# Kernel optimization log

Hardware: AMD Instinct MI355X
Metric: run time of the kernel (lower is better)

The kernel has to match this reference:

```python
import jax, jax.numpy as jnp
import numpy as np

NEG_SLOPE = 0.01  # torch F.leaky_relu default

def _leaky(x):
    return jnp.where(x >= 0, x, NEG_SLOPE * x)

def _gcn(x, W, b, src, dst, w, n):
    # GCNConv(add_self_loops=False, normalize=False):
    # h = x @ W; out[dst] += w * h[src]; out += b
    h = x @ W
    agg = jax.ops.segment_sum(w[:, None] * h[src], dst, num_segments=n)
    return agg + b

def setup_inputs() -> dict:
    key = jax.random.key(0)
    ks = jax.random.split(key, 10)
    N, E, IN, HID, OUT, B = 100000, 300000, 256, 256, 256, 128
    features = jax.random.normal(ks[0], (N, IN), dtype=jnp.float32)
    values = jax.random.uniform(ks[1], (E,), dtype=jnp.float32)
    s = 1.0 / np.sqrt(IN)
    W1 = jax.random.normal(ks[2], (IN, HID), dtype=jnp.float32) * s
    b1 = jnp.zeros((HID,), dtype=jnp.float32)
    W2 = jax.random.normal(ks[3], (HID + IN, OUT), dtype=jnp.float32) * (1.0 / np.sqrt(HID + IN))
    b2 = jnp.zeros((OUT,), dtype=jnp.float32)
    Wl = jax.random.normal(ks[4], (HID + OUT, IN), dtype=jnp.float32) * (1.0 / np.sqrt(HID + OUT))
    bl = jnp.zeros((IN,), dtype=jnp.float32)
    adjs = jax.random.randint(ks[5], (2, E), 0, N, dtype=jnp.int64)
    batch = jnp.sort(jax.random.randint(ks[6], (N,), 0, B, dtype=jnp.int64))
    root_idx = jax.random.randint(ks[7], (B,), 0, N, dtype=jnp.int64)
    return {"features": features, "values": values, "W1": W1, "b1": b1,
            "W2": W2, "b2": b2, "Wl": Wl, "bl": bl,
            "adjs": adjs, "batch": batch, "root_idx": root_idx}

def reference(features, values, W1, b1, W2, b2, Wl, bl, adjs, batch, root_idx):
    N = features.shape[0]
    src, dst = adjs[0], adjs[1]
    f1 = features  # [N, in]
    h = _gcn(f1, W1, b1, src, dst, values, N)  # conv1 -> [N, hid]
    f2 = h
    # root_extend: per-batch broadcast of root features == gather f1[root_idx[batch]]
    root1 = f1[root_idx[batch]]  # [N, in]
    x = _leaky(jnp.concatenate([h, root1], axis=1))
    # dropout is identity at inference
    x = _gcn(x, W2, b2, src, dst, values, N)  # conv2 -> [N, out]
    x = _leaky(x)
    root2 = f2[root_idx[batch]]  # [N, hid]
    x = jnp.concatenate([x, root2], axis=1)
    return _leaky(x @ Wl + bl)  # [N, in]
```

## Files before the change

kernel.cpp:

```cpp
#include <hip/hip_runtime.h>

typedef short short8 __attribute__((ext_vector_type(8)));
typedef float floatx4 __attribute__((ext_vector_type(4)));

#define LEAKY(v) ((v) >= 0.0f ? (v) : 0.01f * (v))

constexpr int D = 256;

__device__ __forceinline__ short f2bf(float x) {
  unsigned u = __float_as_uint(x);
  u += 0x7fffu + ((u >> 16) & 1u);
  return (short)(u >> 16);
}
__device__ __forceinline__ float bf2f(short s) {
  return __uint_as_float(((unsigned)(unsigned short)s) << 16);
}

#define AS1 __attribute__((address_space(1)))
#define AS3 __attribute__((address_space(3)))

__device__ __forceinline__ void gload_lds16(const void* g, void* lds) {
  __builtin_amdgcn_global_load_lds((const AS1 void*)g, (AS3 void*)lds, 16, 0, 0);
}

__global__ void transpose_w(const float* __restrict__ W1,
                            const float* __restrict__ W2,
                            const float* __restrict__ Wl,
                            short* __restrict__ Wt) {
  __shared__ float t[32][33];
  const float* src = (blockIdx.z == 0) ? W1 : (blockIdx.z == 1) ? W2 : Wl;
  short* dst = Wt + (size_t)blockIdx.z * D * D;
  int tx = threadIdx.x, ty = threadIdx.y;
  t[ty][tx] = src[(size_t)(blockIdx.y * 32 + ty) * D + blockIdx.x * 32 + tx];
  __syncthreads();
  dst[(size_t)(blockIdx.x * 32 + ty) * D + blockIdx.y * 32 + tx] =
      f2bf(t[tx][ty]);
}

__global__ __launch_bounds__(256) void conv_bf(const float* __restrict__ X,
                                               short* __restrict__ Y,
                                               long n8) {
  long i = (long)blockIdx.x * 256 + threadIdx.x;
  const long stride = (long)gridDim.x * 256;
  for (; i < n8; i += stride) {
    float4 v0 = ((const float4*)X)[2 * i];
    float4 v1 = ((const float4*)X)[2 * i + 1];
    short8 s;
    s[0] = f2bf(v0.x); s[1] = f2bf(v0.y); s[2] = f2bf(v0.z); s[3] = f2bf(v0.w);
    s[4] = f2bf(v1.x); s[5] = f2bf(v1.y); s[6] = f2bf(v1.z); s[7] = f2bf(v1.w);
    ((short8*)Y)[i] = s;
  }
}

template <bool ADD_ROW, bool FINAL>
__global__ __launch_bounds__(512, 2) void gemm_pipe(
    const short* __restrict__ A, const short* __restrict__ Wt,
    const float* __restrict__ R, const int* __restrict__ batch,
    const float* __restrict__ bias, void* __restrict__ Cvoid, int M,
    int nTiles) {
  __shared__ __align__(16) short As[2][32 * 256];
  const int tid = threadIdx.x;
  const int l = tid & 63, w = tid >> 6, lm = l & 15, q = l >> 4;
  const int ncol0 = w * 32;

  short8 bf[2][8];
#pragma unroll
  for (int j = 0; j < 2; j++)
#pragma unroll
    for (int kk = 0; kk < 8; kk++)
      bf[j][kk] = *(const short8*)(Wt + (size_t)(ncol0 + j * 16 + lm) * D +
                                   kk * 32 + q * 8);
#pragma unroll
  for (int j = 0; j < 2; j++)
#pragma unroll
    for (int kk = 0; kk < 8; kk++)
      asm volatile("" : "+v"(bf[j][kk]));

  float4 b4[2];
  if (FINAL) {
#pragma unroll
    for (int j = 0; j < 2; j++)
      b4[j] = *(const float4*)(bias + ncol0 + j * 16 + q * 4);
  }

  const int stride = gridDim.x;
  int t = blockIdx.x;
  int p = 0;

  auto stage = [&](int tile, int buf) {
#pragma unroll
    for (int r = 0; r < 2; r++) {
      const int s = r * 8 + w;
      const int kk = s >> 1, i = s & 1;
      int grow = tile * 32 + i * 16 + lm;
      grow = grow < M ? grow : M - 1;
      const char* src = (const char*)A + (size_t)grow * 512 + kk * 64 + q * 16;
      gload_lds16(src, (char*)(&As[buf][0]) + s * 1024);
    }
  };

  if (t < nTiles) stage(t, 0);

  for (; t < nTiles; t += stride) {
    __syncthreads();
    const int nxt = t + stride;
    if (nxt < nTiles) stage(nxt, p ^ 1);

    floatx4 acc[2][2];
#pragma unroll
    for (int i = 0; i < 2; i++)
#pragma unroll
      for (int j = 0; j < 2; j++) acc[i][j] = (floatx4){0.f, 0.f, 0.f, 0.f};

    const char* base = (const char*)(&As[p][0]) + (size_t)l * 16;
#pragma unroll
    for (int kk = 0; kk < 8; kk++) {
      short8 a[2];
#pragma unroll
      for (int i = 0; i < 2; i++)
        a[i] = *(const short8*)(base + (kk * 2 + i) * 1024);
#pragma unroll
      for (int i = 0; i < 2; i++)
#pragma unroll
        for (int j = 0; j < 2; j++)
          acc[i][j] = __builtin_amdgcn_mfma_f32_16x16x32_bf16(
              bf[j][kk], a[i], acc[i][j], 0, 0, 0);
    }

    const int rowBase = t * 32;
#pragma unroll
    for (int i = 0; i < 2; i++) {
      const int row = rowBase + i * 16 + lm;
      if (row < M) {
        int rb = 0;
        if (ADD_ROW) rb = batch[row];
#pragma unroll
        for (int j = 0; j < 2; j++) {
          const int col0 = ncol0 + j * 16 + q * 4;
          float c0 = acc[i][j][0], c1 = acc[i][j][1], c2 = acc[i][j][2],
                c3 = acc[i][j][3];
          if (ADD_ROW) {
            float4 rv = *(const float4*)(R + (size_t)rb * D + col0);
            c0 += rv.x; c1 += rv.y; c2 += rv.z; c3 += rv.w;
          }
          if (!FINAL) {
            uint2 o;
            o.x = (unsigned)(unsigned short)f2bf(c0) |
                  ((unsigned)(unsigned short)f2bf(c1) << 16);
            o.y = (unsigned)(unsigned short)f2bf(c2) |
                  ((unsigned)(unsigned short)f2bf(c3) << 16);
            *(uint2*)((short*)Cvoid + (size_t)row * D + col0) = o;
          } else {
            c0 += b4[j].x; c1 += b4[j].y; c2 += b4[j].z; c3 += b4[j].w;
            c0 = LEAKY(c0); c1 = LEAKY(c1); c2 = LEAKY(c2); c3 = LEAKY(c3);
            float4 o = {c0, c1, c2, c3};
            *(float4*)((float*)Cvoid + (size_t)row * D + col0) = o;
          }
        }
      }
    }
    p ^= 1;
  }
}

__global__ void count_dst(const int* __restrict__ dst, int* __restrict__ offs,
                          int E) {
  int e = blockIdx.x * 256 + threadIdx.x;
  if (e < E) atomicAdd(&offs[dst[e]], 1);
}

__global__ void scan_blocks(int* __restrict__ offs, int* __restrict__ bsums,
                            int n) {
  __shared__ int tmp[256];
  int i = blockIdx.x * 256 + threadIdx.x;
  int v = (i < n) ? offs[i] : 0;
  tmp[threadIdx.x] = v;
  __syncthreads();
  for (int off = 1; off < 256; off <<= 1) {
    int t = (threadIdx.x >= off) ? tmp[threadIdx.x - off] : 0;
    __syncthreads();
    tmp[threadIdx.x] += t;
    __syncthreads();
  }
  if (i < n) offs[i] = tmp[threadIdx.x] - v;
  if (threadIdx.x == 255) bsums[blockIdx.x] = tmp[255];
}

__global__ void scan_sums(int* __restrict__ bs, int nb) {
  __shared__ int tmp[1024];
  int v = (threadIdx.x < nb) ? bs[threadIdx.x] : 0;
  tmp[threadIdx.x] = v;
  __syncthreads();
  for (int off = 1; off < 1024; off <<= 1) {
    int t = (threadIdx.x >= off) ? tmp[threadIdx.x - off] : 0;
    __syncthreads();
    tmp[threadIdx.x] += t;
    __syncthreads();
  }
  if (threadIdx.x < nb) bs[threadIdx.x] = tmp[threadIdx.x] - v;
}

__global__ void add_offsets(int* __restrict__ offs, const int* __restrict__ bs,
                            int n, int* __restrict__ cursor) {
  int i = blockIdx.x * 256 + threadIdx.x;
  if (i < n) {
    int o = offs[i] + bs[blockIdx.x];
    offs[i] = o;
    cursor[i] = o;
  }
}

__global__ void fill_buckets(const int* __restrict__ src,
                             const int* __restrict__ dst,
                             const float* __restrict__ vals,
                             int* __restrict__ cursor, int* __restrict__ esrc,
                             float* __restrict__ ew, int E) {
  int e = blockIdx.x * 256 + threadIdx.x;
  if (e < E) {
    int p = atomicAdd(&cursor[dst[e]], 1);
    esrc[p] = src[e];
    ew[p] = vals[e];
  }
}

__global__ __launch_bounds__(256) void aggregate_bf(
    const short* __restrict__ H, const int* __restrict__ offs,
    const int* __restrict__ esrc, const float* __restrict__ ew,
    const float* __restrict__ bias, short* __restrict__ out, int N, int E) {
  int node = blockIdx.x * 4 + (threadIdx.x >> 6);
  if (node >= N) return;
  int lane = threadIdx.x & 63;
  int beg = offs[node];
  int end = (node == N - 1) ? E : offs[node + 1];
  float a0 = 0.f, a1 = 0.f, a2 = 0.f, a3 = 0.f;
  int i = beg;
  for (; i + 1 < end; i += 2) {
    int s0 = esrc[i], s1 = esrc[i + 1];
    float w0 = ew[i], w1 = ew[i + 1];
    uint2 p0 = ((const uint2*)(H + (size_t)s0 * D))[lane];
    uint2 p1 = ((const uint2*)(H + (size_t)s1 * D))[lane];
    a0 += w0 * bf2f((short)(p0.x & 0xffff)) + w1 * bf2f((short)(p1.x & 0xffff));
    a1 += w0 * bf2f((short)(p0.x >> 16))    + w1 * bf2f((short)(p1.x >> 16));
    a2 += w0 * bf2f((short)(p0.y & 0xffff)) + w1 * bf2f((short)(p1.y & 0xffff));
    a3 += w0 * bf2f((short)(p0.y >> 16))    + w1 * bf2f((short)(p1.y >> 16));
  }
  if (i < end) {
    int s = esrc[i];
    float wv = ew[i];
    uint2 pk = ((const uint2*)(H + (size_t)s * D))[lane];
    a0 += wv * bf2f((short)(pk.x & 0xffff));
    a1 += wv * bf2f((short)(pk.x >> 16));
    a2 += wv * bf2f((short)(pk.y & 0xffff));
    a3 += wv * bf2f((short)(pk.y >> 16));
  }
  float4 b = ((const float4*)bias)[lane];
  a0 = LEAKY(a0 + b.x);
  a1 = LEAKY(a1 + b.y);
  a2 = LEAKY(a2 + b.z);
  a3 = LEAKY(a3 + b.w);
  uint2 o;
  o.x = (unsigned)(unsigned short)f2bf(a0) |
        ((unsigned)(unsigned short)f2bf(a1) << 16);
  o.y = (unsigned)(unsigned short)f2bf(a2) |
        ((unsigned)(unsigned short)f2bf(a3) << 16);
  ((uint2*)(out + (size_t)node * D))[lane] = o;
}

__global__ void root_both(const float* __restrict__ X,
                          const int* __restrict__ root_idx,
                          const float* __restrict__ W2, float* __restrict__ R1,
                          const short* __restrict__ H,
                          const int* __restrict__ offs,
                          const int* __restrict__ esrc,
                          const float* __restrict__ ew,
                          const float* __restrict__ b1,
                          const float* __restrict__ Wl, float* __restrict__ R2,
                          int N, int E, int B) {
  __shared__ float a[D];
  int j = threadIdx.x;
  if ((int)blockIdx.x < B) {
    int b = blockIdx.x;
    int r = root_idx[b];
    a[j] = LEAKY(X[(size_t)r * D + j]);
    __syncthreads();
    float acc = 0.f;
#pragma unroll 8
    for (int k = 0; k < D; k++) acc += a[k] * W2[(size_t)(D + k) * D + j];
    R1[b * D + j] = acc;
  } else {
    int b = blockIdx.x - B;
    int r = root_idx[b];
    int beg = offs[r], end = (r == N - 1) ? E : offs[r + 1];
    float acc = b1[j];
    for (int e = beg; e < end; e++)
      acc += ew[e] * bf2f(H[(size_t)esrc[e] * D + j]);
    a[j] = acc;
    __syncthreads();
    float s = 0.f;
#pragma unroll 8
    for (int k = 0; k < D; k++) s += a[k] * Wl[(size_t)(D + k) * D + j];
    R2[b * D + j] = s;
  }
}

extern "C" void kernel_launch(void* const* d_in, const int* in_sizes, int n_in,
                              void* d_out, int out_size, void* d_ws,
                              size_t ws_size, hipStream_t stream) {
  const float* features = (const float*)d_in[0];
  const float* values   = (const float*)d_in[1];
  const float* W1 = (const float*)d_in[2];
  const float* b1 = (const float*)d_in[3];
  const float* W2 = (const float*)d_in[4];
  const float* b2 = (const float*)d_in[5];
  const float* Wl = (const float*)d_in[6];
  const float* bl = (const float*)d_in[7];
  const int* adjs = (const int*)d_in[8];
  const int* batch = (const int*)d_in[9];
  const int* root_idx = (const int*)d_in[10];

  const int N = in_sizes[0] / D;
  const int E = in_sizes[1];
  const int B = in_sizes[10];
  const int* srcI = adjs;
  const int* dstI = adjs + E;

  short* bf0 = (short*)d_ws;
  short* bf1 = bf0 + (size_t)N * D;
  short* Wt = bf1 + (size_t)N * D;
  float* R1 = (float*)(Wt + (size_t)3 * D * D);
  float* R2 = R1 + (size_t)B * D;
  float* ew = R2 + (size_t)B * D;
  int* offs = (int*)(ew + E);
  int* cursor = offs + N;
  int* esrc = cursor + N;
  int* bsums = esrc + E;

  const int nb = (N + 255) / 256;

  hipMemsetAsync(offs, 0, (size_t)N * sizeof(int), stream);
  count_dst<<<(E + 255) / 256, 256, 0, stream>>>(dstI, offs, E);
  scan_blocks<<<nb, 256, 0, stream>>>(offs, bsums, N);
  scan_sums<<<1, 1024, 0, stream>>>(bsums, nb);
  add_offsets<<<nb, 256, 0, stream>>>(offs, bsums, N, cursor);
  fill_buckets<<<(E + 255) / 256, 256, 0, stream>>>(srcI, dstI, values, cursor,
                                                    esrc, ew, E);

  transpose_w<<<dim3(8, 8, 3), dim3(32, 32), 0, stream>>>(W1, W2, Wl, Wt);

  conv_bf<<<2048, 256, 0, stream>>>(features, bf1, (long)N * D / 8);

  const int nTiles = (N + 31) / 32;
  const int ggrid = 512;
  const int aggGrid = (N + 3) / 4;

  gemm_pipe<false, false><<<ggrid, 512, 0, stream>>>(
      bf1, Wt, nullptr, nullptr, nullptr, bf0, N, nTiles);

  aggregate_bf<<<aggGrid, 256, 0, stream>>>(bf0, offs, esrc, ew, b1, bf1, N, E);

  root_both<<<2 * B, 256, 0, stream>>>(features, root_idx, W2, R1, bf0, offs,
                                       esrc, ew, b1, Wl, R2, N, E, B);

  gemm_pipe<true, false><<<ggrid, 512, 0, stream>>>(
      bf1, Wt + (size_t)D * D, R1, batch, nullptr, bf0, N, nTiles);

  aggregate_bf<<<aggGrid, 256, 0, stream>>>(bf0, offs, esrc, ew, b2, bf1, N, E);

  gemm_pipe<true, true><<<ggrid, 512, 0, stream>>>(
      bf1, Wt + (size_t)2 * D * D, R2, batch, bl, (float*)d_out, N, nTiles);
}
```

Before: 434.2 us.

## Fuse fp32-to-bf16 conversion into first GEMM and widen aggregate loads

Removes the separate conversion kernel by letting the first GEMM stream fp32 features straight into LDS and convert them to bf16 when it builds the MFMA operands. This drops a full write and re-read of an N×256 bf16 buffer, but doubles the LDS tile size for that GEMM, which may lower occupancy. The aggregation kernel also now has each half-wave process a different edge with 16-byte loads and combines the two halves with a cross-lane shuffle, so each wave keeps two edge gathers in flight.

```diff
diff --git a/kernel.cpp b/kernel.cpp
--- a/kernel.cpp
+++ b/kernel.cpp
@@ -37,28 +37,14 @@
       f2bf(t[tx][ty]);
 }
 
-__global__ __launch_bounds__(256) void conv_bf(const float* __restrict__ X,
-                                               short* __restrict__ Y,
-                                               long n8) {
-  long i = (long)blockIdx.x * 256 + threadIdx.x;
-  const long stride = (long)gridDim.x * 256;
-  for (; i < n8; i += stride) {
-    float4 v0 = ((const float4*)X)[2 * i];
-    float4 v1 = ((const float4*)X)[2 * i + 1];
-    short8 s;
-    s[0] = f2bf(v0.x); s[1] = f2bf(v0.y); s[2] = f2bf(v0.z); s[3] = f2bf(v0.w);
-    s[4] = f2bf(v1.x); s[5] = f2bf(v1.y); s[6] = f2bf(v1.z); s[7] = f2bf(v1.w);
-    ((short8*)Y)[i] = s;
-  }
-}
-
-template <bool ADD_ROW, bool FINAL>
+template <bool A_F32, bool ADD_ROW, bool FINAL>
 __global__ __launch_bounds__(512, 2) void gemm_pipe(
-    const short* __restrict__ A, const short* __restrict__ Wt,
+    const void* __restrict__ Avoid, const short* __restrict__ Wt,
     const float* __restrict__ R, const int* __restrict__ batch,
     const float* __restrict__ bias, void* __restrict__ Cvoid, int M,
     int nTiles) {
-  __shared__ __align__(16) short As[2][32 * 256];
+  constexpr int TB = A_F32 ? 32768 : 16384;
+  __shared__ __align__(16) char As[2][TB];
   const int tid = threadIdx.x;
   const int l = tid & 63, w = tid >> 6, lm = l & 15, q = l >> 4;
   const int ncol0 = w * 32;
@@ -88,14 +74,29 @@
   int p = 0;
 
   auto stage = [&](int tile, int buf) {
-#pragma unroll
-    for (int r = 0; r < 2; r++) {
-      const int s = r * 8 + w;
-      const int kk = s >> 1, i = s & 1;
-      int grow = tile * 32 + i * 16 + lm;
-      grow = grow < M ? grow : M - 1;
-      const char* src = (const char*)A + (size_t)grow * 512 + kk * 64 + q * 16;
-      gload_lds16(src, (char*)(&As[buf][0]) + s * 1024);
+    if (A_F32) {
+#pragma unroll
+      for (int r = 0; r < 4; r++) {
+        const int c = r * 8 + w;
+        const int s = c >> 1, h = c & 1;
+        const int kk = s >> 1, i = s & 1;
+        int grow = tile * 32 + i * 16 + lm;
+        grow = grow < M ? grow : M - 1;
+        const char* src = (const char*)Avoid + (size_t)grow * 1024 +
+                          kk * 128 + q * 32 + h * 16;
+        gload_lds16(src, &As[buf][s * 2048 + h * 1024]);
+      }
+    } else {
+#pragma unroll
+      for (int r = 0; r < 2; r++) {
+        const int s = r * 8 + w;
+        const int kk = s >> 1, i = s & 1;
+        int grow = tile * 32 + i * 16 + lm;
+        grow = grow < M ? grow : M - 1;
+        const char* src =
+            (const char*)Avoid + (size_t)grow * 512 + kk * 64 + q * 16;
+        gload_lds16(src, &As[buf][s * 1024]);
+      }
     }
   };
 
@@ -112,13 +113,24 @@
 #pragma unroll
       for (int j = 0; j < 2; j++) acc[i][j] = (floatx4){0.f, 0.f, 0.f, 0.f};
 
-    const char* base = (const char*)(&As[p][0]) + (size_t)l * 16;
+    const char* base = &As[p][0] + (size_t)l * 16;
 #pragma unroll
     for (int kk = 0; kk < 8; kk++) {
       short8 a[2];
 #pragma unroll
-      for (int i = 0; i < 2; i++)
-        a[i] = *(const short8*)(base + (kk * 2 + i) * 1024);
+      for (int i = 0; i < 2; i++) {
+        if (A_F32) {
+          const int s = kk * 2 + i;
+          float4 lo = *(const float4*)(base + s * 2048);
+          float4 hi = *(const float4*)(base + s * 2048 + 1024);
+          short8 sv;
+          sv[0] = f2bf(lo.x); sv[1] = f2bf(lo.y); sv[2] = f2bf(lo.z); sv[3] = f2bf(lo.w);
+          sv[4] = f2bf(hi.x); sv[5] = f2bf(hi.y); sv[6] = f2bf(hi.z); sv[7] = f2bf(hi.w);
+          a[i] = sv;
+        } else {
+          a[i] = *(const short8*)(base + (kk * 2 + i) * 1024);
+        }
+      }
 #pragma unroll
       for (int i = 0; i < 2; i++)
 #pragma unroll
@@ -229,41 +241,49 @@
     const float* __restrict__ bias, short* __restrict__ out, int N, int E) {
   int node = blockIdx.x * 4 + (threadIdx.x >> 6);
   if (node >= N) return;
-  int lane = threadIdx.x & 63;
+  const int lane = threadIdx.x & 63;
+  const int half = lane >> 5, li = lane & 31;
   int beg = offs[node];
   int end = (node == N - 1) ? E : offs[node + 1];
-  float a0 = 0.f, a1 = 0.f, a2 = 0.f, a3 = 0.f;
-  int i = beg;
-  for (; i + 1 < end; i += 2) {
-    int s0 = esrc[i], s1 = esrc[i + 1];
-    float w0 = ew[i], w1 = ew[i + 1];
-    uint2 p0 = ((const uint2*)(H + (size_t)s0 * D))[lane];
-    uint2 p1 = ((const uint2*)(H + (size_t)s1 * D))[lane];
-    a0 += w0 * bf2f((short)(p0.x & 0xffff)) + w1 * bf2f((short)(p1.x & 0xffff));
-    a1 += w0 * bf2f((short)(p0.x >> 16))    + w1 * bf2f((short)(p1.x >> 16));
-    a2 += w0 * bf2f((short)(p0.y & 0xffff)) + w1 * bf2f((short)(p1.y & 0xffff));
-    a3 += w0 * bf2f((short)(p0.y >> 16))    + w1 * bf2f((short)(p1.y >> 16));
-  }
-  if (i < end) {
-    int s = esrc[i];
-    float wv = ew[i];
-    uint2 pk = ((const uint2*)(H + (size_t)s * D))[lane];
+  float a0 = 0.f, a1 = 0.f, a2 = 0.f, a3 = 0.f, a4 = 0.f, a5 = 0.f,
+        a6 = 0.f, a7 = 0.f;
+  for (int i = beg; i < end; i += 2) {
+    const int idx = i + half;
+    const bool v = idx < end;
+    int s = esrc[v ? idx : i];
+    float wv = v ? ew[idx] : 0.f;
+    uint4 pk = *(const uint4*)(H + (size_t)s * D + li * 8);
     a0 += wv * bf2f((short)(pk.x & 0xffff));
     a1 += wv * bf2f((short)(pk.x >> 16));
     a2 += wv * bf2f((short)(pk.y & 0xffff));
     a3 += wv * bf2f((short)(pk.y >> 16));
-  }
-  float4 b = ((const float4*)bias)[lane];
-  a0 = LEAKY(a0 + b.x);
-  a1 = LEAKY(a1 + b.y);
-  a2 = LEAKY(a2 + b.z);
-  a3 = LEAKY(a3 + b.w);
-  uint2 o;
-  o.x = (unsigned)(unsigned short)f2bf(a0) |
-        ((unsigned)(unsigned short)f2bf(a1) << 16);
-  o.y = (unsigned)(unsigned short)f2bf(a2) |
-        ((unsigned)(unsigned short)f2bf(a3) << 16);
-  ((uint2*)(out + (size_t)node * D))[lane] = o;
+    a4 += wv * bf2f((short)(pk.z & 0xffff));
+    a5 += wv * bf2f((short)(pk.z >> 16));
+    a6 += wv * bf2f((short)(pk.w & 0xffff));
+    a7 += wv * bf2f((short)(pk.w >> 16));
+  }
+  a0 += __shfl_xor(a0, 32); a1 += __shfl_xor(a1, 32);
+  a2 += __shfl_xor(a2, 32); a3 += __shfl_xor(a3, 32);
+  a4 += __shfl_xor(a4, 32); a5 += __shfl_xor(a5, 32);
+  a6 += __shfl_xor(a6, 32); a7 += __shfl_xor(a7, 32);
+  if (half == 0) {
+    float4 b0 = *(const float4*)(bias + li * 8);
+    float4 b1 = *(const float4*)(bias + li * 8 + 4);
+    a0 = LEAKY(a0 + b0.x); a1 = LEAKY(a1 + b0.y);
+    a2 = LEAKY(a2 + b0.z); a3 = LEAKY(a3 + b0.w);
+    a4 = LEAKY(a4 + b1.x); a5 = LEAKY(a5 + b1.y);
+    a6 = LEAKY(a6 + b1.z); a7 = LEAKY(a7 + b1.w);
+    uint4 o;
+    o.x = (unsigned)(unsigned short)f2bf(a0) |
+          ((unsigned)(unsigned short)f2bf(a1) << 16);
+    o.y = (unsigned)(unsigned short)f2bf(a2) |
+          ((unsigned)(unsigned short)f2bf(a3) << 16);
+    o.z = (unsigned)(unsigned short)f2bf(a4) |
+          ((unsigned)(unsigned short)f2bf(a5) << 16);
+    o.w = (unsigned)(unsigned short)f2bf(a6) |
+          ((unsigned)(unsigned short)f2bf(a7) << 16);
+    *(uint4*)(out + (size_t)node * D + li * 8) = o;
+  }
 }
 
 __global__ void root_both(const float* __restrict__ X,
@@ -347,25 +367,23 @@
 
   transpose_w<<<dim3(8, 8, 3), dim3(32, 32), 0, stream>>>(W1, W2, Wl, Wt);
 
-  conv_bf<<<2048, 256, 0, stream>>>(features, bf1, (long)N * D / 8);
-
   const int nTiles = (N + 31) / 32;
   const int ggrid = 512;
   const int aggGrid = (N + 3) / 4;
 
-  gemm_pipe<false, false><<<ggrid, 512, 0, stream>>>(
-      bf1, Wt, nullptr, nullptr, nullptr, bf0, N, nTiles);
+  gemm_pipe<true, false, false><<<ggrid, 512, 0, stream>>>(
+      features, Wt, nullptr, nullptr, nullptr, bf0, N, nTiles);
 
   aggregate_bf<<<aggGrid, 256, 0, stream>>>(bf0, offs, esrc, ew, b1, bf1, N, E);
 
   root_both<<<2 * B, 256, 0, stream>>>(features, root_idx, W2, R1, bf0, offs,
                                        esrc, ew, b1, Wl, R2, N, E, B);
 
-  gemm_pipe<true, false><<<ggrid, 512, 0, stream>>>(
+  gemm_pipe<false, true, false><<<ggrid, 512, 0, stream>>>(
       bf1, Wt + (size_t)D * D, R1, batch, nullptr, bf0, N, nTiles);
 
   aggregate_bf<<<aggGrid, 256, 0, stream>>>(bf0, offs, esrc, ew, b2, bf1, N, E);
 
-  gemm_pipe<true, true><<<ggrid, 512, 0, stream>>>(
+  gemm_pipe<false, true, true><<<ggrid, 512, 0, stream>>>(
       bf1, Wt + (size_t)2 * D * D, R2, batch, bl, (float*)d_out, N, nTiles);
 }
```

Result: faster. 419.1 us (-3.5%).
